# Kernel tuning notes

Measured on AMD Instinct MI355X. Metric: run time of the kernel, lower is better.

## Reference

```python
import jax, jax.numpy as jnp
import numpy as np

IN_C, HID, L, NN, BS, OUT = 32, 128, 4, 64, 512, 3
N = NN * BS  # total graph vertices
EPS_LN = 1e-5
EPS_SM = 1e-16  # PyG softmax eps


def setup_inputs() -> dict:
    key = jax.random.key(0)
    ks = jax.random.split(key, 16)
    E = 524288
    x = jax.random.normal(ks[0], (N, IN_C), dtype=jnp.float32)
    edge_index = jax.random.randint(ks[1], (2, E), 0, N, dtype=jnp.int64)
    s = 0.1
    # first GAT layer (in -> hidden)
    W0 = jax.random.normal(ks[2], (IN_C, HID), dtype=jnp.float32) * s
    att_src0 = jax.random.normal(ks[3], (HID,), dtype=jnp.float32) * s
    att_dst0 = jax.random.normal(ks[4], (HID,), dtype=jnp.float32) * s
    bias0 = jnp.zeros((HID,), dtype=jnp.float32)
    # residual GAT layers (hidden -> hidden), stacked over L
    W_res = jax.random.normal(ks[5], (L, HID, HID), dtype=jnp.float32) * s
    att_src_res = jax.random.normal(ks[6], (L, HID), dtype=jnp.float32) * s
    att_dst_res = jax.random.normal(ks[7], (L, HID), dtype=jnp.float32) * s
    bias_res = jnp.zeros((L, HID), dtype=jnp.float32)
    gamma = jnp.ones((L, HID), dtype=jnp.float32)
    beta = jnp.zeros((L, HID), dtype=jnp.float32)
    # per-node predictor heads
    W1p = jax.random.normal(ks[8], (NN, HID, HID // 2), dtype=jnp.float32) * s
    W2p = jax.random.normal(ks[9], (NN, HID // 2, OUT), dtype=jnp.float32) * s
    return {"x": x, "edge_index": edge_index, "W0": W0, "att_src0": att_src0,
            "att_dst0": att_dst0, "bias0": bias0, "W_res": W_res,
            "att_src_res": att_src_res, "att_dst_res": att_dst_res,
            "bias_res": bias_res, "gamma": gamma, "beta": beta,
            "W1p": W1p, "W2p": W2p}


def _gat(x, src, dst, W, a_src, a_dst, b):
    # PyG GATConv, heads=1, negative_slope=0.2, self-loops already appended
    h = x @ W                                   # [N, H]
    a_s = (h * a_src).sum(-1)                   # [N]
    a_d = (h * a_dst).sum(-1)                   # [N]
    e = jax.nn.leaky_relu(a_s[src] + a_d[dst], 0.2)   # [E]
    m = jax.ops.segment_max(e, dst, num_segments=N)
    e = jnp.exp(e - m[dst])
    z = jax.ops.segment_sum(e, dst, num_segments=N)
    alpha = e / (z[dst] + EPS_SM)               # [E]
    out = jax.ops.segment_sum(h[src] * alpha[:, None], dst, num_segments=N)
    return out + b


def _layernorm(x, g, b):
    mu = x.mean(-1, keepdims=True)
    var = ((x - mu) ** 2).mean(-1, keepdims=True)
    return (x - mu) * jax.lax.rsqrt(var + EPS_LN) * g + b


def reference(x, edge_index, W0, att_src0, att_dst0, bias0, W_res,
              att_src_res, att_dst_res, bias_res, gamma, beta, W1p, W2p):
    loops = jnp.arange(N, dtype=edge_index.dtype)
    src = jnp.concatenate([edge_index[0], loops])
    dst = jnp.concatenate([edge_index[1], loops])
    # first GAT + relu
    h = jax.nn.relu(_gat(x, src, dst, W0, att_src0, att_dst0, bias0))
    # res+ blocks: h = h + conv(dropout(act(norm(h))))  (dropout=identity, eval)
    for i in range(L):
        t = jax.nn.relu(_layernorm(h, gamma[i], beta[i]))
        t = _gat(t, src, dst, W_res[i], att_src_res[i], att_dst_res[i], bias_res[i])
        h = h + t
    h = jax.nn.relu(_layernorm(h, gamma[0], beta[0]))
    # per-node predictor heads
    h = h.reshape(NN, BS, HID)
    t = jax.nn.relu(jnp.einsum('nbh,nhk->nbk', h, W1p))
    logits = jnp.einsum('nbk,nko->nbo', t, W2p)
    return jax.nn.softmax(logits, axis=-1)   # softmax over class dim (dim=1 per node slice)
```

## Files before the change

### kernel.cpp

```cpp
#include <hip/hip_runtime.h>
#include <hip/hip_fp8.h>
#include <math.h>

#define NND   32768
#define HIDD  128
#define NHEAD 64
#define BSS   512
#define OUTC  3

typedef _Float16 half_t;
typedef __attribute__((ext_vector_type(8))) _Float16 half8;
typedef __attribute__((ext_vector_type(4))) float f32x4;

__device__ __forceinline__ unsigned enc_fp8x4(float a, float b, float c, float d) {
    __hip_fp8x4_e4m3 q(make_float4(a, b, c, d));
    return (unsigned)q.__x;
}
__device__ __forceinline__ float4 dec_fp8x4(unsigned v) {
    __hip_fp8x4_e4m3 t; t.__x = (__hip_fp8x4_storage_t)v;
    return (float4)t;
}

__global__ __launch_bounds__(256) void prep_kernel(const float* __restrict__ W0,
        const float* __restrict__ W_res, const float* __restrict__ W1p,
// ... 77 lines not shown
    int tmp[32];
    int run = 0;
#pragma unroll
    for (int i = 0; i < 8; ++i) {
        int4 c4 = *(const int4*)&counts[base + i * 4];
        tmp[i*4+0] = run; run += c4.x;
        tmp[i*4+1] = run; run += c4.y;
        tmp[i*4+2] = run; run += c4.z;
        tmp[i*4+3] = run; run += c4.w;
    }
    sums[tid] = run;
    __syncthreads();
    for (int d = 1; d < 1024; d <<= 1) {
        int v = (tid >= d) ? sums[tid - d] : 0;
        __syncthreads();
        sums[tid] += v;
        __syncthreads();
    }
    int ebase = (tid == 0) ? 0 : sums[tid - 1];
#pragma unroll
    for (int i = 0; i < 32; ++i) off[base + i] = ebase + tmp[i];
    if (tid == 1023) off[NND] = sums[1023];
}

__global__ __launch_bounds__(256) void fill_a0_kernel(const int* __restrict__ ei, int E, int egrid,
        const int* __restrict__ off, const int* __restrict__ rank, int* __restrict__ csr_src,
        const half_t* __restrict__ xh, const float* __restrict__ wvec,
        float* __restrict__ a_s, float* __restrict__ a_d) {
    int b = blockIdx.x, tid = threadIdx.x;
    if (b < egrid) {
        int j = b * 256 + tid;
        int Etot = E + NND;
        if (j >= Etot) return;
        int src, dst;
        if (j < E) { src = ei[j]; dst = ei[E + j]; }
        else       { src = j - E; dst = j - E; }
        csr_src[off[dst] + rank[j]] = src;
    } else {
        __shared__ float ws0[32], wd0[32];
        if (tid < 32) { ws0[tid] = wvec[tid]; wd0[tid] = wvec[640 + tid]; }
        __syncthreads();
        int g = (b - egrid) * 256 + tid;
        int node = g >> 2, part = g & 3;
        half8 xv = *(const half8*)&xh[(size_t)node * 32 + part * 8];
        float s = 0.f, d2 = 0.f;
#pragma unroll
        for (int j = 0; j < 8; ++j) { float f = (float)xv[j]; s += f * ws0[part * 8 + j]; d2 += f * wd0[part * 8 + j]; }
        s += __shfl_xor(s, 1); s += __shfl_xor(s, 2);
        d2 += __shfl_xor(d2, 1); d2 += __shfl_xor(d2, 2);
        if (part == 0) { a_s[node] = s; a_d[node] = d2; }
    }
}

__global__ __launch_bounds__(256) void agg0_kernel(const half_t* __restrict__ xh,
        const float* __restrict__ a_s, const float* __restrict__ a_dv,
        const int* __restrict__ csr_src, const int* __restrict__ off,
        half_t* __restrict__ P) {
    int d = (blockIdx.x * 256 + threadIdx.x) >> 6;
    int lane = threadIdx.x & 63;
    int q = lane >> 4, r15 = lane & 15;
    int beg = off[d], end = off[d + 1];
    float adv = a_dv[d];
    float pz = 0.f, a0 = 0.f, a1 = 0.f;
    for (int base = beg; base < end; base += 64) {
        int j = base + lane;
        int s = 0; float p = 0.f;
        if (j < end) {
            s = csr_src[j];
            float t = a_s[s] + adv;
            t = (t > 0.f) ? t : 0.2f * t;
            p = __expf(t);
        }
        pz += p;
        int cnt = end - base; if (cnt > 64) cnt = 64;
        int full = cnt & ~15;
        int k4 = 0;
        for (; k4 < full; k4 += 16) {
            int s0 = __shfl(s, k4 + q);      float p0 = __shfl(p, k4 + q);
            int s1 = __shfl(s, k4 + 4 + q);  float p1 = __shfl(p, k4 + 4 + q);
            int s2 = __shfl(s, k4 + 8 + q);  float p2 = __shfl(p, k4 + 8 + q);
            int s3 = __shfl(s, k4 + 12 + q); float p3 = __shfl(p, k4 + 12 + q);
            union { unsigned u; half_t h[2]; } u0, u1, u2, u3;
            u0.u = *(const unsigned*)&xh[(size_t)s0 * 32 + r15 * 2];
            u1.u = *(const unsigned*)&xh[(size_t)s1 * 32 + r15 * 2];
            u2.u = *(const unsigned*)&xh[(size_t)s2 * 32 + r15 * 2];
            u3.u = *(const unsigned*)&xh[(size_t)s3 * 32 + r15 * 2];
            a0 += p0 * (float)u0.h[0] + p1 * (float)u1.h[0] + p2 * (float)u2.h[0] + p3 * (float)u3.h[0];
            a1 += p0 * (float)u0.h[1] + p1 * (float)u1.h[1] + p2 * (float)u2.h[1] + p3 * (float)u3.h[1];
        }
        for (; k4 < cnt; k4 += 4) {
            int s0 = __shfl(s, k4 + q); float p0 = __shfl(p, k4 + q);
            union { unsigned u; half_t h[2]; } u0;
            u0.u = *(const unsigned*)&xh[(size_t)s0 * 32 + r15 * 2];
            a0 += p0 * (float)u0.h[0]; a1 += p0 * (float)u0.h[1];
        }
    }
#pragma unroll
    for (int o = 32; o; o >>= 1) pz += __shfl_xor(pz, o);
    a0 += __shfl_xor(a0, 16); a0 += __shfl_xor(a0, 32);
    a1 += __shfl_xor(a1, 16); a1 += __shfl_xor(a1, 32);
    if (q == 0) {
        float inv = 1.f / (pz + 1e-16f);
        union { unsigned u; half_t h[2]; } w;
        w.h[0] = (half_t)(a0 * inv); w.h[1] = (half_t)(a1 * inv);
        *(unsigned*)&P[(size_t)d * 32 + r15 * 2] = w.u;
    }
}

__global__ __launch_bounds__(256) void agg_kernel(const unsigned char* __restrict__ F8,
        const float* __restrict__ a_s, const float* __restrict__ a_dv,
        const int* __restrict__ csr_src, const int* __restrict__ off,
        half_t* __restrict__ P) {
    int d = (blockIdx.x * 256 + threadIdx.x) >> 6;
    int lane = threadIdx.x & 63;
    int q = lane >> 4, r15 = lane & 15;
    int beg = off[d], end = off[d + 1];
    float adv = a_dv[d];
    float pz = 0.f;
    float acc[8] = {0.f,0.f,0.f,0.f,0.f,0.f,0.f,0.f};
    for (int base = beg; base < end; base += 64) {
        int j = base + lane;
        int s = 0; float p = 0.f;
        if (j < end) {
            s = csr_src[j];
            float t = a_s[s] + adv;
            t = (t > 0.f) ? t : 0.2f * t;
            p = __expf(t);
        }
        pz += p;
        int cnt = end - base; if (cnt > 64) cnt = 64;
        int full = cnt & ~15;
        int k4 = 0;
        for (; k4 < full; k4 += 16) {
            int s0 = __shfl(s, k4 + q);      float p0 = __shfl(p, k4 + q);
            int s1 = __shfl(s, k4 + 4 + q);  float p1 = __shfl(p, k4 + 4 + q);
            int s2 = __shfl(s, k4 + 8 + q);  float p2 = __shfl(p, k4 + 8 + q);
            int s3 = __shfl(s, k4 + 12 + q); float p3 = __shfl(p, k4 + 12 + q);
            uint2 r0 = *(const uint2*)&F8[(size_t)s0 * HIDD + r15 * 8];
            uint2 r1 = *(const uint2*)&F8[(size_t)s1 * HIDD + r15 * 8];
            uint2 r2 = *(const uint2*)&F8[(size_t)s2 * HIDD + r15 * 8];
            uint2 r3 = *(const uint2*)&F8[(size_t)s3 * HIDD + r15 * 8];
            float4 f;
            f = dec_fp8x4(r0.x); acc[0]+=p0*f.x; acc[1]+=p0*f.y; acc[2]+=p0*f.z; acc[3]+=p0*f.w;
            f = dec_fp8x4(r0.y); acc[4]+=p0*f.x; acc[5]+=p0*f.y; acc[6]+=p0*f.z; acc[7]+=p0*f.w;
            f = dec_fp8x4(r1.x); acc[0]+=p1*f.x; acc[1]+=p1*f.y; acc[2]+=p1*f.z; acc[3]+=p1*f.w;
            f = dec_fp8x4(r1.y); acc[4]+=p1*f.x; acc[5]+=p1*f.y; acc[6]+=p1*f.z; acc[7]+=p1*f.w;
            f = dec_fp8x4(r2.x); acc[0]+=p2*f.x; acc[1]+=p2*f.y; acc[2]+=p2*f.z; acc[3]+=p2*f.w;
            f = dec_fp8x4(r2.y); acc[4]+=p2*f.x; acc[5]+=p2*f.y; acc[6]+=p2*f.z; acc[7]+=p2*f.w;
            f = dec_fp8x4(r3.x); acc[0]+=p3*f.x; acc[1]+=p3*f.y; acc[2]+=p3*f.z; acc[3]+=p3*f.w;
            f = dec_fp8x4(r3.y); acc[4]+=p3*f.x; acc[5]+=p3*f.y; acc[6]+=p3*f.z; acc[7]+=p3*f.w;
        }
        for (; k4 < cnt; k4 += 4) {
            int s0 = __shfl(s, k4 + q); float p0 = __shfl(p, k4 + q);
            uint2 r0 = *(const uint2*)&F8[(size_t)s0 * HIDD + r15 * 8];
            float4 f;
            f = dec_fp8x4(r0.x); acc[0]+=p0*f.x; acc[1]+=p0*f.y; acc[2]+=p0*f.z; acc[3]+=p0*f.w;
            f = dec_fp8x4(r0.y); acc[4]+=p0*f.x; acc[5]+=p0*f.y; acc[6]+=p0*f.z; acc[7]+=p0*f.w;
        }
    }
#pragma unroll
    for (int o = 32; o; o >>= 1) pz += __shfl_xor(pz, o);
#pragma unroll
    for (int i = 0; i < 8; ++i) {
        acc[i] += __shfl_xor(acc[i], 16);
        acc[i] += __shfl_xor(acc[i], 32);
    }
    if (q == 0) {
        float inv = 1.f / (pz + 1e-16f);
        union { int4 v; half_t hh[8]; } u;
#pragma unroll
        for (int i = 0; i < 8; ++i) u.hh[i] = (half_t)(acc[i] * inv);
        *(int4*)&P[(size_t)d * HIDD + r15 * 8] = u.v;
    }
}

template <int K, bool RES>
__global__ __launch_bounds__(256) void gemm_kernel(const half_t* __restrict__ P,
        const half_t* __restrict__ Whl, const float* __restrict__ bias,
        half_t* __restrict__ Hh, unsigned char* __restrict__ Th8,
        const float* __restrict__ gamma, const float* __restrict__ beta,
        const float* __restrict__ wsn, const float* __restrict__ wdn,
        float* __restrict__ a_s, float* __restrict__ a_d) {
    constexpr int KP = K + 8;
    constexpr int WB = 128 * KP * 2;
    constexpr int VB = 64 * 132 * 4;
    __shared__ __align__(16) char smraw[(WB > VB) ? WB : VB];
    half_t* w = (half_t*)smraw;
    float* vv = (float*)smraw;
    int tid = threadIdx.x;
    int n0 = blockIdx.x * 64;
    for (int i = tid; i < 128 * (K / 8); i += 256) {
        int n = i / (K / 8), c = i % (K / 8);
        *(int4*)&w[n * KP + c * 8] = *(const int4*)&Whl[(size_t)n * K + c * 8];
    }
    int wv = tid >> 6, lane = tid & 63;
    int q = lane >> 4, r15 = lane & 15;
    half8 afrag[K / 32];
    int nodeA = n0 + wv * 16 + r15;
#pragma unroll
    for (int s = 0; s < K / 32; ++s)
        afrag[s] = *(const half8*)&P[(size_t)nodeA * K + s * 32 + q * 8];
    __syncthreads();
    f32x4 acc[8];
#pragma unroll
    for (int ct = 0; ct < 8; ++ct) {
        f32x4 c = {0.f, 0.f, 0.f, 0.f};
#pragma unroll
        for (int s = 0; s < K / 32; ++s) {
            half8 bfrag = *(const half8*)&w[(ct * 16 + r15) * KP + s * 32 + q * 8];
            c = __builtin_amdgcn_mfma_f32_16x16x32_f16(afrag[s], bfrag, c, 0, 0, 0);
        }
        acc[ct] = c;
    }
    __syncthreads();
#pragma unroll
    for (int ct = 0; ct < 8; ++ct)
#pragma unroll
        for (int r = 0; r < 4; ++r)
            vv[(wv * 16 + q * 4 + r) * 132 + ct * 16 + r15] = acc[ct][r];
    __syncthreads();
    int grp = tid >> 4, sub = tid & 15;
    float4 bi0 = *(const float4*)&bias[sub * 8],  bi1 = *(const float4*)&bias[sub * 8 + 4];
    float4 g0  = *(const float4*)&gamma[sub * 8], g1  = *(const float4*)&gamma[sub * 8 + 4];
    float4 be0 = *(const float4*)&beta[sub * 8],  be1 = *(const float4*)&beta[sub * 8 + 4];
    float4 ws0 = *(const float4*)&wsn[sub * 8],   ws1 = *(const float4*)&wsn[sub * 8 + 4];
    float4 wd0 = *(const float4*)&wdn[sub * 8],   wd1 = *(const float4*)&wdn[sub * 8 + 4];
    float bi[8] = {bi0.x,bi0.y,bi0.z,bi0.w,bi1.x,bi1.y,bi1.z,bi1.w};
    float gg[8] = {g0.x,g0.y,g0.z,g0.w,g1.x,g1.y,g1.z,g1.w};
    float be[8] = {be0.x,be0.y,be0.z,be0.w,be1.x,be1.y,be1.z,be1.w};
    float ws[8] = {ws0.x,ws0.y,ws0.z,ws0.w,ws1.x,ws1.y,ws1.z,ws1.w};
    float wd[8] = {wd0.x,wd0.y,wd0.z,wd0.w,wd1.x,wd1.y,wd1.z,wd1.w};
#pragma unroll
    for (int pp = 0; pp < 4; ++pp) {
        int nl = grp + pp * 16;
        int node = n0 + nl;
        float v8[8];
#pragma unroll
        for (int j = 0; j < 8; ++j) v8[j] = vv[nl * 132 + sub * 8 + j] + bi[j];
        if (RES) {
            half8 hold = *(const half8*)&Hh[(size_t)node * HIDD + sub * 8];
#pragma unroll
            for (int j = 0; j < 8; ++j) v8[j] += (float)hold[j];
        } else {
#pragma unroll
            for (int j = 0; j < 8; ++j) v8[j] = fmaxf(v8[j], 0.f);
        }
        union { int4 i4; half_t h[8]; } hw;
#pragma unroll
        for (int j = 0; j < 8; ++j) hw.h[j] = (half_t)v8[j];
        *(int4*)&Hh[(size_t)node * HIDD + sub * 8] = hw.i4;
        float sum = 0.f;
#pragma unroll
        for (int j = 0; j < 8; ++j) sum += v8[j];
#pragma unroll
        for (int o = 8; o; o >>= 1) sum += __shfl_xor(sum, o);
        float mu = sum * (1.f / HIDD);
        float var = 0.f;
#pragma unroll
        for (int j = 0; j < 8; ++j) { float dx = v8[j] - mu; var += dx * dx; }
#pragma unroll
        for (int o = 8; o; o >>= 1) var += __shfl_xor(var, o);
        float rs = rsqrtf(var * (1.f / HIDD) + 1e-5f);
        float tt[8];
        float asn = 0.f, adn = 0.f;
#pragma unroll
        for (int j = 0; j < 8; ++j) {
            float t = fmaxf((v8[j] - mu) * rs * gg[j] + be[j], 0.f);
            tt[j] = t;
            asn += t * ws[j];
            adn += t * wd[j];
        }
        uint2 tw;
        tw.x = enc_fp8x4(tt[0], tt[1], tt[2], tt[3]);
        tw.y = enc_fp8x4(tt[4], tt[5], tt[6], tt[7]);
        *(uint2*)&Th8[(size_t)node * HIDD + sub * 8] = tw;
#pragma unroll
        for (int o = 8; o; o >>= 1) { asn += __shfl_xor(asn, o); adn += __shfl_xor(adn, o); }
        if (sub == 0) { a_s[node] = asn; a_d[node] = adn; }
    }
}

__global__ __launch_bounds__(256) void gemm_last_kernel(const half_t* __restrict__ P,
        const half_t* __restrict__ Whl, const float* __restrict__ bias,
        const half_t* __restrict__ Hh,
        const float* __restrict__ gamma, const float* __restrict__ beta,
        const half_t* __restrict__ W1h, const float* __restrict__ W2p,
        float* __restrict__ out) {
    __shared__ __align__(16) char smraw[128 * 136 * 2];
    half_t* w = (half_t*)smraw;
    float* vv = (float*)smraw;
    int tid = threadIdx.x;
    int n0 = blockIdx.x * 64;
    for (int i = tid; i < 128 * 16; i += 256) {
        int n = i >> 4, c = i & 15;
        *(int4*)&w[n * 136 + c * 8] = *(const int4*)&Whl[(size_t)n * 128 + c * 8];
    }
    int wv = tid >> 6, lane = tid & 63;
    int q = lane >> 4, r15 = lane & 15;
    half8 afrag[4];
    int nodeA = n0 + wv * 16 + r15;
#pragma unroll
    for (int s = 0; s < 4; ++s)
        afrag[s] = *(const half8*)&P[(size_t)nodeA * HIDD + s * 32 + q * 8];
    __syncthreads();
    f32x4 acc[8];
#pragma unroll
    for (int ct = 0; ct < 8; ++ct) {
        f32x4 c = {0.f, 0.f, 0.f, 0.f};
#pragma unroll
        for (int s = 0; s < 4; ++s) {
            half8 bfrag = *(const half8*)&w[(ct * 16 + r15) * 136 + s * 32 + q * 8];
            c = __builtin_amdgcn_mfma_f32_16x16x32_f16(afrag[s], bfrag, c, 0, 0, 0);
        }
        acc[ct] = c;
    }
    __syncthreads();
#pragma unroll
    for (int ct = 0; ct < 8; ++ct)
#pragma unroll
        for (int r = 0; r < 4; ++r)
            vv[(wv * 16 + q * 4 + r) * 132 + ct * 16 + r15] = acc[ct][r];
    __syncthreads();
    int grp = tid >> 4, sub = tid & 15;
    float4 bi0 = *(const float4*)&bias[sub * 8],  bi1 = *(const float4*)&bias[sub * 8 + 4];
    float4 g0  = *(const float4*)&gamma[sub * 8], g1  = *(const float4*)&gamma[sub * 8 + 4];
    float4 be0 = *(const float4*)&beta[sub * 8],  be1 = *(const float4*)&beta[sub * 8 + 4];
    float bi[8] = {bi0.x,bi0.y,bi0.z,bi0.w,bi1.x,bi1.y,bi1.z,bi1.w};
    float gg[8] = {g0.x,g0.y,g0.z,g0.w,g1.x,g1.y,g1.z,g1.w};
    float be[8] = {be0.x,be0.y,be0.z,be0.w,be1.x,be1.y,be1.z,be1.w};
    half_t tv[4][8];
#pragma unroll
    for (int pp = 0; pp < 4; ++pp) {
        int nl = grp + pp * 16;
        int node = n0 + nl;
        float v8[8];
        half8 hold = *(const half8*)&Hh[(size_t)node * HIDD + sub * 8];
#pragma unroll
        for (int j = 0; j < 8; ++j) v8[j] = vv[nl * 132 + sub * 8 + j] + bi[j] + (float)hold[j];
        float sum = 0.f;
#pragma unroll
        for (int j = 0; j < 8; ++j) sum += v8[j];
#pragma unroll
        for (int o = 8; o; o >>= 1) sum += __shfl_xor(sum, o);
        float mu = sum * (1.f / HIDD);
        float var = 0.f;
#pragma unroll
        for (int j = 0; j < 8; ++j) { float dx = v8[j] - mu; var += dx * dx; }
#pragma unroll
        for (int o = 8; o; o >>= 1) var += __shfl_xor(var, o);
        float rs = rsqrtf(var * (1.f / HIDD) + 1e-5f);
#pragma unroll
        for (int j = 0; j < 8; ++j)
            tv[pp][j] = (half_t)fmaxf((v8[j] - mu) * rs * gg[j] + be[j], 0.f);
    }
    __syncthreads();
#pragma unroll
    for (int pp = 0; pp < 4; ++pp) {
        int nl = grp + pp * 16;
        union { int4 i4; half_t h[8]; } u;
#pragma unroll
        for (int j = 0; j < 8; ++j) u.h[j] = tv[pp][j];
        *(int4*)&w[nl * 136 + sub * 8] = u.i4;
    }
    __syncthreads();
    int head = n0 >> 9;
    const half_t* W1g = W1h + (size_t)head * 64 * 128;
    half8 pa[4];
#pragma unroll
    for (int s = 0; s < 4; ++s)
        pa[s] = *(const half8*)&w[(wv * 16 + r15) * 136 + s * 32 + q * 8];
    float lg[3][4];
#pragma unroll
    for (int o = 0; o < 3; ++o)
#pragma unroll
        for (int r = 0; r < 4; ++r) lg[o][r] = 0.f;
#pragma unroll
    for (int ct2 = 0; ct2 < 4; ++ct2) {
        int n2 = ct2 * 16 + r15;
        f32x4 c = {0.f, 0.f, 0.f, 0.f};
#pragma unroll
        for (int s = 0; s < 4; ++s) {
            half8 bfrag = *(const half8*)&W1g[(size_t)n2 * 128 + s * 32 + q * 8];
            c = __builtin_amdgcn_mfma_f32_16x16x32_f16(pa[s], bfrag, c, 0, 0, 0);
        }
        float w2a = W2p[(size_t)head * 192 + n2 * 3 + 0];
        float w2b = W2p[(size_t)head * 192 + n2 * 3 + 1];
        float w2c = W2p[(size_t)head * 192 + n2 * 3 + 2];
#pragma unroll
        for (int r = 0; r < 4; ++r) {
            float t = fmaxf(c[r], 0.f);
            lg[0][r] += t * w2a;
            lg[1][r] += t * w2b;
            lg[2][r] += t * w2c;
        }
    }
#pragma unroll
    for (int o = 8; o; o >>= 1)
#pragma unroll
        for (int oo = 0; oo < 3; ++oo)
#pragma unroll
            for (int r = 0; r < 4; ++r) lg[oo][r] += __shfl_xor(lg[oo][r], o);
    if (r15 == 0) {
        int nodeD = n0 + wv * 16 + q * 4;
#pragma unroll
        for (int r = 0; r < 4; ++r) {
            float l0 = lg[0][r], l1 = lg[1][r], l2 = lg[2][r];
            float mx = fmaxf(l0, fmaxf(l1, l2));
            float e0 = __expf(l0 - mx), e1 = __expf(l1 - mx), e2 = __expf(l2 - mx);
            float inv = 1.f / (e0 + e1 + e2);
            float* op = out + (size_t)(nodeD + r) * OUTC;
            op[0] = e0 * inv; op[1] = e1 * inv; op[2] = e2 * inv;
        }
    }
}

extern "C" void kernel_launch(void* const* d_in, const int* in_sizes, int n_in,
                              void* d_out, int out_size, void* d_ws, size_t ws_size,
                              hipStream_t stream) {
    const float* x        = (const float*)d_in[0];
    const int*   ei       = (const int*)d_in[1];
    const float* W0       = (const float*)d_in[2];
    const float* att_src0 = (const float*)d_in[3];
    const float* att_dst0 = (const float*)d_in[4];
    const float* bias0    = (const float*)d_in[5];
    const float* W_res    = (const float*)d_in[6];
    const float* as_res   = (const float*)d_in[7];
    const float* ad_res   = (const float*)d_in[8];
    const float* b_res    = (const float*)d_in[9];
    const float* gamma    = (const float*)d_in[10];
    const float* beta     = (const float*)d_in[11];
    const float* W1p      = (const float*)d_in[12];
    const float* W2p      = (const float*)d_in[13];
    float* out = (float*)d_out;

    int E = in_sizes[1] / 2;
    int Etot = E + NND;

    char* p = (char*)d_ws;
    auto alloc = [&](size_t bytes) { void* r = (void*)p; p += (bytes + 255) & ~(size_t)255; return r; };
    int*    counts  = (int*)alloc((size_t)NND * 4);
    int*    off     = (int*)alloc((size_t)(NND + 1) * 4);
    int*    rank    = (int*)alloc((size_t)Etot * 4);
    int*    csr_src = (int*)alloc((size_t)Etot * 4);
    half_t* xh      = (half_t*)alloc((size_t)NND * 32 * 2);
    half_t* Pbuf    = (half_t*)alloc((size_t)NND * HIDD * 2);
    unsigned char* Th8 = (unsigned char*)alloc((size_t)NND * HIDD);
    half_t* Hh      = (half_t*)alloc((size_t)NND * HIDD * 2);
    float*  a_s     = (float*)alloc((size_t)NND * 4);
    float*  a_d     = (float*)alloc((size_t)NND * 4);
    half_t* Wh      = (half_t*)alloc((size_t)4 * HIDD * HIDD * 2);
    half_t* W1h     = (half_t*)alloc((size_t)NHEAD * 64 * HIDD * 2);
    half_t* W0t     = (half_t*)alloc((size_t)HIDD * 32 * 2);
    float*  wvec    = (float*)alloc((size_t)1280 * 4);

    int egrid = (Etot + 255) / 256;

    hipMemsetAsync(counts, 0, (size_t)NND * 4, stream);
    prep_kernel<<<1090 + egrid, 256, 0, stream>>>(W0, W_res, W1p, att_src0, att_dst0,
        as_res, ad_res, x, ei, E, Wh, W1h, W0t, wvec, xh, counts, rank);
    scan_kernel<<<1, 1024, 0, stream>>>(counts, off);
    fill_a0_kernel<<<egrid + 512, 256, 0, stream>>>(ei, E, egrid, off, rank, csr_src,
                                                    xh, wvec, a_s, a_d);

    agg0_kernel<<<NND / 4, 256, 0, stream>>>(xh, a_s, a_d, csr_src, off, Pbuf);
    gemm_kernel<32, false><<<NND / 64, 256, 0, stream>>>(Pbuf, W0t, bias0, Hh, Th8,
        gamma, beta, wvec + 128, wvec + 640 + 128, a_s, a_d);

    for (int i = 0; i < 3; ++i) {
        agg_kernel<<<NND / 4, 256, 0, stream>>>(Th8, a_s, a_d, csr_src, off, Pbuf);
        gemm_kernel<128, true><<<NND / 64, 256, 0, stream>>>(Pbuf, Wh + (size_t)i * 16384,
            b_res + i * HIDD, Hh, Th8,
            gamma + (i + 1) * HIDD, beta + (i + 1) * HIDD,
            wvec + (i + 2) * 128, wvec + 640 + (i + 2) * 128, a_s, a_d);
    }

    agg_kernel<<<NND / 4, 256, 0, stream>>>(Th8, a_s, a_d, csr_src, off, Pbuf);
    gemm_last_kernel<<<NND / 64, 256, 0, stream>>>(Pbuf, Wh + (size_t)3 * 16384,
        b_res + 3 * HIDD, Hh, gamma, beta, W1h, W2p, out);
}
```

Measured before the change: 281.2 us.

## Fuse GAT aggregation with per-layer GEMM into single 1024-thread layer kernels

```diff
diff --git a/kernel.cpp b/kernel.cpp
--- a/kernel.cpp
+++ b/kernel.cpp
@@ -153,199 +153,113 @@
     }
 }
 
-__global__ __launch_bounds__(256) void agg0_kernel(const half_t* __restrict__ xh,
-        const float* __restrict__ a_s, const float* __restrict__ a_dv,
+__global__ __launch_bounds__(1024, 4) void layer0_kernel(const half_t* __restrict__ xh,
+        const float* __restrict__ asv, const float* __restrict__ adval,
         const int* __restrict__ csr_src, const int* __restrict__ off,
-        half_t* __restrict__ P) {
-    int d = (blockIdx.x * 256 + threadIdx.x) >> 6;
-    int lane = threadIdx.x & 63;
-    int q = lane >> 4, r15 = lane & 15;
-    int beg = off[d], end = off[d + 1];
-    float adv = a_dv[d];
-    float pz = 0.f, a0 = 0.f, a1 = 0.f;
-    for (int base = beg; base < end; base += 64) {
-        int j = base + lane;
-        int s = 0; float p = 0.f;
-        if (j < end) {
-            s = csr_src[j];
-            float t = a_s[s] + adv;
-            t = (t > 0.f) ? t : 0.2f * t;
-            p = __expf(t);
-        }
-        pz += p;
-        int cnt = end - base; if (cnt > 64) cnt = 64;
-        int full = cnt & ~15;
-        int k4 = 0;
-        for (; k4 < full; k4 += 16) {
-            int s0 = __shfl(s, k4 + q);      float p0 = __shfl(p, k4 + q);
-            int s1 = __shfl(s, k4 + 4 + q);  float p1 = __shfl(p, k4 + 4 + q);
-            int s2 = __shfl(s, k4 + 8 + q);  float p2 = __shfl(p, k4 + 8 + q);
-            int s3 = __shfl(s, k4 + 12 + q); float p3 = __shfl(p, k4 + 12 + q);
-            union { unsigned u; half_t h[2]; } u0, u1, u2, u3;
-            u0.u = *(const unsigned*)&xh[(size_t)s0 * 32 + r15 * 2];
-            u1.u = *(const unsigned*)&xh[(size_t)s1 * 32 + r15 * 2];
-            u2.u = *(const unsigned*)&xh[(size_t)s2 * 32 + r15 * 2];
-            u3.u = *(const unsigned*)&xh[(size_t)s3 * 32 + r15 * 2];
-            a0 += p0 * (float)u0.h[0] + p1 * (float)u1.h[0] + p2 * (float)u2.h[0] + p3 * (float)u3.h[0];
-            a1 += p0 * (float)u0.h[1] + p1 * (float)u1.h[1] + p2 * (float)u2.h[1] + p3 * (float)u3.h[1];
-        }
-        for (; k4 < cnt; k4 += 4) {
-            int s0 = __shfl(s, k4 + q); float p0 = __shfl(p, k4 + q);
-            union { unsigned u; half_t h[2]; } u0;
-            u0.u = *(const unsigned*)&xh[(size_t)s0 * 32 + r15 * 2];
-            a0 += p0 * (float)u0.h[0]; a1 += p0 * (float)u0.h[1];
-        }
-    }
-#pragma unroll
-    for (int o = 32; o; o >>= 1) pz += __shfl_xor(pz, o);
-    a0 += __shfl_xor(a0, 16); a0 += __shfl_xor(a0, 32);
-    a1 += __shfl_xor(a1, 16); a1 += __shfl_xor(a1, 32);
-    if (q == 0) {
-        float inv = 1.f / (pz + 1e-16f);
-        union { unsigned u; half_t h[2]; } w;
-        w.h[0] = (half_t)(a0 * inv); w.h[1] = (half_t)(a1 * inv);
-        *(unsigned*)&P[(size_t)d * 32 + r15 * 2] = w.u;
-    }
-}
-
-__global__ __launch_bounds__(256) void agg_kernel(const unsigned char* __restrict__ F8,
-        const float* __restrict__ a_s, const float* __restrict__ a_dv,
-        const int* __restrict__ csr_src, const int* __restrict__ off,
-        half_t* __restrict__ P) {
-    int d = (blockIdx.x * 256 + threadIdx.x) >> 6;
-    int lane = threadIdx.x & 63;
-    int q = lane >> 4, r15 = lane & 15;
-    int beg = off[d], end = off[d + 1];
-    float adv = a_dv[d];
-    float pz = 0.f;
-    float acc[8] = {0.f,0.f,0.f,0.f,0.f,0.f,0.f,0.f};
-    for (int base = beg; base < end; base += 64) {
-        int j = base + lane;
-        int s = 0; float p = 0.f;
-        if (j < end) {
-            s = csr_src[j];
-            float t = a_s[s] + adv;
-            t = (t > 0.f) ? t : 0.2f * t;
-            p = __expf(t);
-        }
-        pz += p;
-        int cnt = end - base; if (cnt > 64) cnt = 64;
-        int full = cnt & ~15;
-        int k4 = 0;
-        for (; k4 < full; k4 += 16) {
-            int s0 = __shfl(s, k4 + q);      float p0 = __shfl(p, k4 + q);
-            int s1 = __shfl(s, k4 + 4 + q);  float p1 = __shfl(p, k4 + 4 + q);
-            int s2 = __shfl(s, k4 + 8 + q);  float p2 = __shfl(p, k4 + 8 + q);
-            int s3 = __shfl(s, k4 + 12 + q); float p3 = __shfl(p, k4 + 12 + q);
-            uint2 r0 = *(const uint2*)&F8[(size_t)s0 * HIDD + r15 * 8];
-            uint2 r1 = *(const uint2*)&F8[(size_t)s1 * HIDD + r15 * 8];
-            uint2 r2 = *(const uint2*)&F8[(size_t)s2 * HIDD + r15 * 8];
-            uint2 r3 = *(const uint2*)&F8[(size_t)s3 * HIDD + r15 * 8];
-            float4 f;
-            f = dec_fp8x4(r0.x); acc[0]+=p0*f.x; acc[1]+=p0*f.y; acc[2]+=p0*f.z; acc[3]+=p0*f.w;
-            f = dec_fp8x4(r0.y); acc[4]+=p0*f.x; acc[5]+=p0*f.y; acc[6]+=p0*f.z; acc[7]+=p0*f.w;
-            f = dec_fp8x4(r1.x); acc[0]+=p1*f.x; acc[1]+=p1*f.y; acc[2]+=p1*f.z; acc[3]+=p1*f.w;
-            f = dec_fp8x4(r1.y); acc[4]+=p1*f.x; acc[5]+=p1*f.y; acc[6]+=p1*f.z; acc[7]+=p1*f.w;
-            f = dec_fp8x4(r2.x); acc[0]+=p2*f.x; acc[1]+=p2*f.y; acc[2]+=p2*f.z; acc[3]+=p2*f.w;
-            f = dec_fp8x4(r2.y); acc[4]+=p2*f.x; acc[5]+=p2*f.y; acc[6]+=p2*f.z; acc[7]+=p2*f.w;
-            f = dec_fp8x4(r3.x); acc[0]+=p3*f.x; acc[1]+=p3*f.y; acc[2]+=p3*f.z; acc[3]+=p3*f.w;
-            f = dec_fp8x4(r3.y); acc[4]+=p3*f.x; acc[5]+=p3*f.y; acc[6]+=p3*f.z; acc[7]+=p3*f.w;
-        }
-        for (; k4 < cnt; k4 += 4) {
-            int s0 = __shfl(s, k4 + q); float p0 = __shfl(p, k4 + q);
-            uint2 r0 = *(const uint2*)&F8[(size_t)s0 * HIDD + r15 * 8];
-            float4 f;
-            f = dec_fp8x4(r0.x); acc[0]+=p0*f.x; acc[1]+=p0*f.y; acc[2]+=p0*f.z; acc[3]+=p0*f.w;
-            f = dec_fp8x4(r0.y); acc[4]+=p0*f.x; acc[5]+=p0*f.y; acc[6]+=p0*f.z; acc[7]+=p0*f.w;
-        }
-    }
-#pragma unroll
-    for (int o = 32; o; o >>= 1) pz += __shfl_xor(pz, o);
-#pragma unroll
-    for (int i = 0; i < 8; ++i) {
-        acc[i] += __shfl_xor(acc[i], 16);
-        acc[i] += __shfl_xor(acc[i], 32);
-    }
-    if (q == 0) {
-        float inv = 1.f / (pz + 1e-16f);
-        union { int4 v; half_t hh[8]; } u;
-#pragma unroll
-        for (int i = 0; i < 8; ++i) u.hh[i] = (half_t)(acc[i] * inv);
-        *(int4*)&P[(size_t)d * HIDD + r15 * 8] = u.v;
-    }
-}
-
-template <int K, bool RES>
-__global__ __launch_bounds__(256) void gemm_kernel(const half_t* __restrict__ P,
-        const half_t* __restrict__ Whl, const float* __restrict__ bias,
-        half_t* __restrict__ Hh, unsigned char* __restrict__ Th8,
+        const half_t* __restrict__ W0t, const float* __restrict__ bias,
+        half_t* __restrict__ Hh,
         const float* __restrict__ gamma, const float* __restrict__ beta,
+        unsigned char* __restrict__ Th8o,
         const float* __restrict__ wsn, const float* __restrict__ wdn,
-        float* __restrict__ a_s, float* __restrict__ a_d) {
-    constexpr int KP = K + 8;
-    constexpr int WB = 128 * KP * 2;
-    constexpr int VB = 64 * 132 * 4;
-    __shared__ __align__(16) char smraw[(WB > VB) ? WB : VB];
-    half_t* w = (half_t*)smraw;
-    float* vv = (float*)smraw;
-    int tid = threadIdx.x;
-    int n0 = blockIdx.x * 64;
-    for (int i = tid; i < 128 * (K / 8); i += 256) {
-        int n = i / (K / 8), c = i % (K / 8);
-        *(int4*)&w[n * KP + c * 8] = *(const int4*)&Whl[(size_t)n * K + c * 8];
-    }
-    int wv = tid >> 6, lane = tid & 63;
-    int q = lane >> 4, r15 = lane & 15;
-    half8 afrag[K / 32];
-    int nodeA = n0 + wv * 16 + r15;
-#pragma unroll
-    for (int s = 0; s < K / 32; ++s)
-        afrag[s] = *(const half8*)&P[(size_t)nodeA * K + s * 32 + q * 8];
+        float* __restrict__ aso, float* __restrict__ ado) {
+    __shared__ __align__(16) char smem[32768];
+    half_t* Wt = (half_t*)smem;
+    half_t* Ps = (half_t*)(smem + 10240);
+    float*  vv = (float*)smem;
+    const int tid = threadIdx.x;
+    const int w = tid >> 6, lane = tid & 63, q = lane >> 4, r15 = lane & 15;
+    const int n0 = blockIdx.x * 128;
+    for (int i = tid; i < 512; i += 1024) {
+        int n = i >> 2, c = i & 3;
+        *(int4*)&Wt[n * 40 + c * 8] = *(const int4*)&W0t[(size_t)n * 32 + c * 8];
+    }
+    for (int t = 0; t < 8; ++t) {
+        int d = n0 + w * 8 + t;
+        int beg = off[d], end = off[d + 1];
+        float adv = adval[d];
+        float pz = 0.f, a0 = 0.f, a1 = 0.f;
+        for (int base = beg; base < end; base += 64) {
+            int j = base + lane;
+            int s = 0; float p = 0.f;
+            if (j < end) {
+                s = csr_src[j];
+                float tt = asv[s] + adv;
+                tt = (tt > 0.f) ? tt : 0.2f * tt;
+                p = __expf(tt);
+            }
+            pz += p;
+            int cnt = end - base; if (cnt > 64) cnt = 64;
+            int full = cnt & ~15;
+            int k4 = 0;
+            for (; k4 < full; k4 += 16) {
+                int s0 = __shfl(s, k4 + q);      float p0 = __shfl(p, k4 + q);
+                int s1 = __shfl(s, k4 + 4 + q);  float p1 = __shfl(p, k4 + 4 + q);
+                int s2 = __shfl(s, k4 + 8 + q);  float p2 = __shfl(p, k4 + 8 + q);
+                int s3 = __shfl(s, k4 + 12 + q); float p3 = __shfl(p, k4 + 12 + q);
+                union { unsigned u; half_t h[2]; } u0, u1, u2, u3;
+                u0.u = *(const unsigned*)&xh[(size_t)s0 * 32 + r15 * 2];
+                u1.u = *(const unsigned*)&xh[(size_t)s1 * 32 + r15 * 2];
+                u2.u = *(const unsigned*)&xh[(size_t)s2 * 32 + r15 * 2];
+                u3.u = *(const unsigned*)&xh[(size_t)s3 * 32 + r15 * 2];
+                a0 += p0 * (float)u0.h[0] + p1 * (float)u1.h[0] + p2 * (float)u2.h[0] + p3 * (float)u3.h[0];
+                a1 += p0 * (float)u0.h[1] + p1 * (float)u1.h[1] + p2 * (float)u2.h[1] + p3 * (float)u3.h[1];
+            }
+            for (; k4 < cnt; k4 += 4) {
+                int s0 = __shfl(s, k4 + q); float p0 = __shfl(p, k4 + q);
+                union { unsigned u; half_t h[2]; } u0;
+                u0.u = *(const unsigned*)&xh[(size_t)s0 * 32 + r15 * 2];
+                a0 += p0 * (float)u0.h[0]; a1 += p0 * (float)u0.h[1];
+            }
+        }
+#pragma unroll
+        for (int o = 32; o; o >>= 1) pz += __shfl_xor(pz, o);
+        a0 += __shfl_xor(a0, 16); a0 += __shfl_xor(a0, 32);
+        a1 += __shfl_xor(a1, 16); a1 += __shfl_xor(a1, 32);
+        if (q == 0) {
+            float inv = 1.f / (pz + 1e-16f);
+            union { unsigned u; half_t h[2]; } uu;
+            uu.h[0] = (half_t)(a0 * inv); uu.h[1] = (half_t)(a1 * inv);
+            *(unsigned*)&Ps[(w * 8 + t) * 40 + r15 * 2] = uu.u;
+        }
+    }
     __syncthreads();
-    f32x4 acc[8];
-#pragma unroll
-    for (int ct = 0; ct < 8; ++ct) {
+    const int rt = w >> 1, cb = (w & 1) * 4;
+    half8 af = *(const half8*)&Ps[(rt * 16 + r15) * 40 + q * 8];
+    f32x4 c4[4];
+#pragma unroll
+    for (int ct = 0; ct < 4; ++ct) {
         f32x4 c = {0.f, 0.f, 0.f, 0.f};
-#pragma unroll
-        for (int s = 0; s < K / 32; ++s) {
-            half8 bfrag = *(const half8*)&w[(ct * 16 + r15) * KP + s * 32 + q * 8];
-            c = __builtin_amdgcn_mfma_f32_16x16x32_f16(afrag[s], bfrag, c, 0, 0, 0);
-        }
-        acc[ct] = c;
+        half8 bf = *(const half8*)&Wt[((cb + ct) * 16 + r15) * 40 + q * 8];
+        c = __builtin_amdgcn_mfma_f32_16x16x32_f16(af, bf, c, 0, 0, 0);
+        c4[ct] = c;
     }
     __syncthreads();
-#pragma unroll
-    for (int ct = 0; ct < 8; ++ct)
-#pragma unroll
-        for (int r = 0; r < 4; ++r)
-            vv[(wv * 16 + q * 4 + r) * 132 + ct * 16 + r15] = acc[ct][r];
-    __syncthreads();
-    int grp = tid >> 4, sub = tid & 15;
+    const int nl = tid >> 4, sub = tid & 15;
     float4 bi0 = *(const float4*)&bias[sub * 8],  bi1 = *(const float4*)&bias[sub * 8 + 4];
     float4 g0  = *(const float4*)&gamma[sub * 8], g1  = *(const float4*)&gamma[sub * 8 + 4];
     float4 be0 = *(const float4*)&beta[sub * 8],  be1 = *(const float4*)&beta[sub * 8 + 4];
-    float4 ws0 = *(const float4*)&wsn[sub * 8],   ws1 = *(const float4*)&wsn[sub * 8 + 4];
-    float4 wd0 = *(const float4*)&wdn[sub * 8],   wd1 = *(const float4*)&wdn[sub * 8 + 4];
+    float4 wsa = *(const float4*)&wsn[sub * 8],   wsb = *(const float4*)&wsn[sub * 8 + 4];
+    float4 wda = *(const float4*)&wdn[sub * 8],   wdb = *(const float4*)&wdn[sub * 8 + 4];
     float bi[8] = {bi0.x,bi0.y,bi0.z,bi0.w,bi1.x,bi1.y,bi1.z,bi1.w};
     float gg[8] = {g0.x,g0.y,g0.z,g0.w,g1.x,g1.y,g1.z,g1.w};
     float be[8] = {be0.x,be0.y,be0.z,be0.w,be1.x,be1.y,be1.z,be1.w};
-    float ws[8] = {ws0.x,ws0.y,ws0.z,ws0.w,ws1.x,ws1.y,ws1.z,ws1.w};
-    float wd[8] = {wd0.x,wd0.y,wd0.z,wd0.w,wd1.x,wd1.y,wd1.z,wd1.w};
-#pragma unroll
-    for (int pp = 0; pp < 4; ++pp) {
-        int nl = grp + pp * 16;
-        int node = n0 + nl;
+    float wsr[8] = {wsa.x,wsa.y,wsa.z,wsa.w,wsb.x,wsb.y,wsb.z,wsb.w};
+    float wdr[8] = {wda.x,wda.y,wda.z,wda.w,wdb.x,wdb.y,wdb.z,wdb.w};
+#pragma unroll
+    for (int chunk = 0; chunk < 2; ++chunk) {
+        if ((rt >> 2) == chunk) {
+            int rb = (rt & 3) * 16 + q * 4;
+#pragma unroll
+            for (int ct = 0; ct < 4; ++ct)
+#pragma unroll
+                for (int r = 0; r < 4; ++r)
+                    vv[(rb + r) * 128 + (cb + ct) * 16 + r15] = c4[ct][r];
+        }
+        __syncthreads();
+        int node = n0 + chunk * 64 + nl;
         float v8[8];
 #pragma unroll
-        for (int j = 0; j < 8; ++j) v8[j] = vv[nl * 132 + sub * 8 + j] + bi[j];
-        if (RES) {
-            half8 hold = *(const half8*)&Hh[(size_t)node * HIDD + sub * 8];
-#pragma unroll
-            for (int j = 0; j < 8; ++j) v8[j] += (float)hold[j];
-        } else {
-#pragma unroll
-            for (int j = 0; j < 8; ++j) v8[j] = fmaxf(v8[j], 0.f);
-        }
+        for (int j = 0; j < 8; ++j) v8[j] = fmaxf(vv[nl * 128 + sub * 8 + j] + bi[j], 0.f);
         union { int4 i4; half_t h[8]; } hw;
 #pragma unroll
         for (int j = 0; j < 8; ++j) hw.h[j] = (half_t)v8[j];
@@ -367,77 +281,155 @@
 #pragma unroll
         for (int j = 0; j < 8; ++j) {
             float t = fmaxf((v8[j] - mu) * rs * gg[j] + be[j], 0.f);
-            tt[j] = t;
-            asn += t * ws[j];
-            adn += t * wd[j];
+            tt[j] = t; asn += t * wsr[j]; adn += t * wdr[j];
         }
         uint2 tw;
         tw.x = enc_fp8x4(tt[0], tt[1], tt[2], tt[3]);
         tw.y = enc_fp8x4(tt[4], tt[5], tt[6], tt[7]);
-        *(uint2*)&Th8[(size_t)node * HIDD + sub * 8] = tw;
+        *(uint2*)&Th8o[(size_t)node * HIDD + sub * 8] = tw;
 #pragma unroll
         for (int o = 8; o; o >>= 1) { asn += __shfl_xor(asn, o); adn += __shfl_xor(adn, o); }
-        if (sub == 0) { a_s[node] = asn; a_d[node] = adn; }
-    }
-}
-
-__global__ __launch_bounds__(256) void gemm_last_kernel(const half_t* __restrict__ P,
+        if (sub == 0) { aso[node] = asn; ado[node] = adn; }
+        __syncthreads();
+    }
+}
+
+template <bool LAST>
+__global__ __launch_bounds__(1024, 4) void layer_kernel(const unsigned char* __restrict__ F8,
+        const float* __restrict__ asv, const float* __restrict__ adval,
+        const int* __restrict__ csr_src, const int* __restrict__ off,
         const half_t* __restrict__ Whl, const float* __restrict__ bias,
-        const half_t* __restrict__ Hh,
+        half_t* __restrict__ Hh,
         const float* __restrict__ gamma, const float* __restrict__ beta,
+        unsigned char* __restrict__ Th8o,
+        const float* __restrict__ wsn, const float* __restrict__ wdn,
+        float* __restrict__ aso, float* __restrict__ ado,
         const half_t* __restrict__ W1h, const float* __restrict__ W2p,
         float* __restrict__ out) {
-    __shared__ __align__(16) char smraw[128 * 136 * 2];
-    half_t* w = (half_t*)smraw;
-    float* vv = (float*)smraw;
-    int tid = threadIdx.x;
-    int n0 = blockIdx.x * 64;
-    for (int i = tid; i < 128 * 16; i += 256) {
+    __shared__ __align__(16) char smem[65536];
+    half_t* Wt = (half_t*)smem;
+    half_t* Ps = (half_t*)(smem + 32768);
+    float*  vv = (float*)smem;
+    const int tid = threadIdx.x;
+    const int w = tid >> 6, lane = tid & 63, q = lane >> 4, r15 = lane & 15;
+    const int n0 = blockIdx.x * 128;
+    for (int i = tid; i < 2048; i += 1024) {
         int n = i >> 4, c = i & 15;
-        *(int4*)&w[n * 136 + c * 8] = *(const int4*)&Whl[(size_t)n * 128 + c * 8];
-    }
-    int wv = tid >> 6, lane = tid & 63;
-    int q = lane >> 4, r15 = lane & 15;
-    half8 afrag[4];
-    int nodeA = n0 + wv * 16 + r15;
-#pragma unroll
-    for (int s = 0; s < 4; ++s)
-        afrag[s] = *(const half8*)&P[(size_t)nodeA * HIDD + s * 32 + q * 8];
+        *(int4*)&Wt[n * 128 + ((c ^ (n & 15)) * 8)] = *(const int4*)&Whl[(size_t)n * 128 + c * 8];
+    }
+    for (int t = 0; t < 8; ++t) {
+        int d = n0 + w * 8 + t;
+        int beg = off[d], end = off[d + 1];
+        float adv = adval[d];
+        float pz = 0.f;
+        float acc[8] = {0.f,0.f,0.f,0.f,0.f,0.f,0.f,0.f};
+        for (int base = beg; base < end; base += 64) {
+            int j = base + lane;
+            int s = 0; float p = 0.f;
+            if (j < end) {
+                s = csr_src[j];
+                float tt = asv[s] + adv;
+                tt = (tt > 0.f) ? tt : 0.2f * tt;
+                p = __expf(tt);
+            }
+            pz += p;
+            int cnt = end - base; if (cnt > 64) cnt = 64;
+            int full = cnt & ~15;
+            int k4 = 0;
+            for (; k4 < full; k4 += 16) {
+                int s0 = __shfl(s, k4 + q);      float p0 = __shfl(p, k4 + q);
+                int s1 = __shfl(s, k4 + 4 + q);  float p1 = __shfl(p, k4 + 4 + q);
+                int s2 = __shfl(s, k4 + 8 + q);  float p2 = __shfl(p, k4 + 8 + q);
+                int s3 = __shfl(s, k4 + 12 + q); float p3 = __shfl(p, k4 + 12 + q);
+                uint2 r0 = *(const uint2*)&F8[(size_t)s0 * HIDD + r15 * 8];
+                uint2 r1 = *(const uint2*)&F8[(size_t)s1 * HIDD + r15 * 8];
+                uint2 r2 = *(const uint2*)&F8[(size_t)s2 * HIDD + r15 * 8];
+                uint2 r3 = *(const uint2*)&F8[(size_t)s3 * HIDD + r15 * 8];
+                float4 f;
+                f = dec_fp8x4(r0.x); acc[0]+=p0*f.x; acc[1]+=p0*f.y; acc[2]+=p0*f.z; acc[3]+=p0*f.w;
+                f = dec_fp8x4(r0.y); acc[4]+=p0*f.x; acc[5]+=p0*f.y; acc[6]+=p0*f.z; acc[7]+=p0*f.w;
+                f = dec_fp8x4(r1.x); acc[0]+=p1*f.x; acc[1]+=p1*f.y; acc[2]+=p1*f.z; acc[3]+=p1*f.w;
+                f = dec_fp8x4(r1.y); acc[4]+=p1*f.x; acc[5]+=p1*f.y; acc[6]+=p1*f.z; acc[7]+=p1*f.w;
+                f = dec_fp8x4(r2.x); acc[0]+=p2*f.x; acc[1]+=p2*f.y; acc[2]+=p2*f.z; acc[3]+=p2*f.w;
+                f = dec_fp8x4(r2.y); acc[4]+=p2*f.x; acc[5]+=p2*f.y; acc[6]+=p2*f.z; acc[7]+=p2*f.w;
+                f = dec_fp8x4(r3.x); acc[0]+=p3*f.x; acc[1]+=p3*f.y; acc[2]+=p3*f.z; acc[3]+=p3*f.w;
+                f = dec_fp8x4(r3.y); acc[4]+=p3*f.x; acc[5]+=p3*f.y; acc[6]+=p3*f.z; acc[7]+=p3*f.w;
+            }
+            for (; k4 < cnt; k4 += 4) {
+                int s0 = __shfl(s, k4 + q); float p0 = __shfl(p, k4 + q);
+                uint2 r0 = *(const uint2*)&F8[(size_t)s0 * HIDD + r15 * 8];
+                float4 f;
+                f = dec_fp8x4(r0.x); acc[0]+=p0*f.x; acc[1]+=p0*f.y; acc[2]+=p0*f.z; acc[3]+=p0*f.w;
+                f = dec_fp8x4(r0.y); acc[4]+=p0*f.x; acc[5]+=p0*f.y; acc[6]+=p0*f.z; acc[7]+=p0*f.w;
+            }
+        }
+#pragma unroll
+        for (int o = 32; o; o >>= 1) pz += __shfl_xor(pz, o);
+#pragma unroll
+        for (int i = 0; i < 8; ++i) {
+            acc[i] += __shfl_xor(acc[i], 16);
+            acc[i] += __shfl_xor(acc[i], 32);
+        }
+        if (q == 0) {
+            float inv = 1.f / (pz + 1e-16f);
+            union { int4 v; half_t hh[8]; } u;
+#pragma unroll
+            for (int i = 0; i < 8; ++i) u.hh[i] = (half_t)(acc[i] * inv);
+            int m = w * 8 + t;
+            *(int4*)&Ps[m * 128 + ((r15 ^ (m & 15)) * 8)] = u.v;
+        }
+    }
     __syncthreads();
-    f32x4 acc[8];
-#pragma unroll
-    for (int ct = 0; ct < 8; ++ct) {
+    const int rt = w >> 1, cb = (w & 1) * 4;
+    half8 af[4];
+#pragma unroll
+    for (int s = 0; s < 4; ++s) {
+        int n = rt * 16 + r15, idx = s * 4 + q;
+        af[s] = *(const half8*)&Ps[n * 128 + ((idx ^ (n & 15)) * 8)];
+    }
+    f32x4 c4[4];
+#pragma unroll
+    for (int ct = 0; ct < 4; ++ct) {
         f32x4 c = {0.f, 0.f, 0.f, 0.f};
+        int n = (cb + ct) * 16 + r15;
 #pragma unroll
         for (int s = 0; s < 4; ++s) {
-            half8 bfrag = *(const half8*)&w[(ct * 16 + r15) * 136 + s * 32 + q * 8];
-            c = __builtin_amdgcn_mfma_f32_16x16x32_f16(afrag[s], bfrag, c, 0, 0, 0);
-        }
-        acc[ct] = c;
+            int idx = s * 4 + q;
+            half8 bf = *(const half8*)&Wt[n * 128 + ((idx ^ (n & 15)) * 8)];
+            c = __builtin_amdgcn_mfma_f32_16x16x32_f16(af[s], bf, c, 0, 0, 0);
+        }
+        c4[ct] = c;
     }
     __syncthreads();
-#pragma unroll
-    for (int ct = 0; ct < 8; ++ct)
-#pragma unroll
-        for (int r = 0; r < 4; ++r)
-            vv[(wv * 16 + q * 4 + r) * 132 + ct * 16 + r15] = acc[ct][r];
-    __syncthreads();
-    int grp = tid >> 4, sub = tid & 15;
+    const int nl = tid >> 4, sub = tid & 15;
     float4 bi0 = *(const float4*)&bias[sub * 8],  bi1 = *(const float4*)&bias[sub * 8 + 4];
     float4 g0  = *(const float4*)&gamma[sub * 8], g1  = *(const float4*)&gamma[sub * 8 + 4];
     float4 be0 = *(const float4*)&beta[sub * 8],  be1 = *(const float4*)&beta[sub * 8 + 4];
     float bi[8] = {bi0.x,bi0.y,bi0.z,bi0.w,bi1.x,bi1.y,bi1.z,bi1.w};
     float gg[8] = {g0.x,g0.y,g0.z,g0.w,g1.x,g1.y,g1.z,g1.w};
     float be[8] = {be0.x,be0.y,be0.z,be0.w,be1.x,be1.y,be1.z,be1.w};
-    half_t tv[4][8];
-#pragma unroll
-    for (int pp = 0; pp < 4; ++pp) {
-        int nl = grp + pp * 16;
-        int node = n0 + nl;
+#pragma unroll
+    for (int chunk = 0; chunk < 2; ++chunk) {
+        if ((rt >> 2) == chunk) {
+            int rb = (rt & 3) * 16 + q * 4;
+#pragma unroll
+            for (int ct = 0; ct < 4; ++ct)
+#pragma unroll
+                for (int r = 0; r < 4; ++r)
+                    vv[(rb + r) * 128 + (cb + ct) * 16 + r15] = c4[ct][r];
+        }
+        __syncthreads();
+        int node = n0 + chunk * 64 + nl;
         float v8[8];
         half8 hold = *(const half8*)&Hh[(size_t)node * HIDD + sub * 8];
 #pragma unroll
-        for (int j = 0; j < 8; ++j) v8[j] = vv[nl * 132 + sub * 8 + j] + bi[j] + (float)hold[j];
+        for (int j = 0; j < 8; ++j) v8[j] = vv[nl * 128 + sub * 8 + j] + bi[j] + (float)hold[j];
+        if (!LAST) {
+            union { int4 i4; half_t h[8]; } hw;
+#pragma unroll
+            for (int j = 0; j < 8; ++j) hw.h[j] = (half_t)v8[j];
+            *(int4*)&Hh[(size_t)node * HIDD + sub * 8] = hw.i4;
+        }
         float sum = 0.f;
 #pragma unroll
         for (int j = 0; j < 8; ++j) sum += v8[j];
@@ -450,67 +442,88 @@
 #pragma unroll
         for (int o = 8; o; o >>= 1) var += __shfl_xor(var, o);
         float rs = rsqrtf(var * (1.f / HIDD) + 1e-5f);
-#pragma unroll
-        for (int j = 0; j < 8; ++j)
-            tv[pp][j] = (half_t)fmaxf((v8[j] - mu) * rs * gg[j] + be[j], 0.f);
-    }
-    __syncthreads();
-#pragma unroll
-    for (int pp = 0; pp < 4; ++pp) {
-        int nl = grp + pp * 16;
-        union { int4 i4; half_t h[8]; } u;
-#pragma unroll
-        for (int j = 0; j < 8; ++j) u.h[j] = tv[pp][j];
-        *(int4*)&w[nl * 136 + sub * 8] = u.i4;
-    }
-    __syncthreads();
-    int head = n0 >> 9;
-    const half_t* W1g = W1h + (size_t)head * 64 * 128;
-    half8 pa[4];
-#pragma unroll
-    for (int s = 0; s < 4; ++s)
-        pa[s] = *(const half8*)&w[(wv * 16 + r15) * 136 + s * 32 + q * 8];
-    float lg[3][4];
-#pragma unroll
-    for (int o = 0; o < 3; ++o)
-#pragma unroll
-        for (int r = 0; r < 4; ++r) lg[o][r] = 0.f;
-#pragma unroll
-    for (int ct2 = 0; ct2 < 4; ++ct2) {
-        int n2 = ct2 * 16 + r15;
-        f32x4 c = {0.f, 0.f, 0.f, 0.f};
-#pragma unroll
-        for (int s = 0; s < 4; ++s) {
-            half8 bfrag = *(const half8*)&W1g[(size_t)n2 * 128 + s * 32 + q * 8];
-            c = __builtin_amdgcn_mfma_f32_16x16x32_f16(pa[s], bfrag, c, 0, 0, 0);
-        }
-        float w2a = W2p[(size_t)head * 192 + n2 * 3 + 0];
-        float w2b = W2p[(size_t)head * 192 + n2 * 3 + 1];
-        float w2c = W2p[(size_t)head * 192 + n2 * 3 + 2];
-#pragma unroll
-        for (int r = 0; r < 4; ++r) {
-            float t = fmaxf(c[r], 0.f);
-            lg[0][r] += t * w2a;
-            lg[1][r] += t * w2b;
-            lg[2][r] += t * w2c;
-        }
-    }
-#pragma unroll
-    for (int o = 8; o; o >>= 1)
-#pragma unroll
-        for (int oo = 0; oo < 3; ++oo)
-#pragma unroll
-            for (int r = 0; r < 4; ++r) lg[oo][r] += __shfl_xor(lg[oo][r], o);
-    if (r15 == 0) {
-        int nodeD = n0 + wv * 16 + q * 4;
-#pragma unroll
-        for (int r = 0; r < 4; ++r) {
-            float l0 = lg[0][r], l1 = lg[1][r], l2 = lg[2][r];
-            float mx = fmaxf(l0, fmaxf(l1, l2));
-            float e0 = __expf(l0 - mx), e1 = __expf(l1 - mx), e2 = __expf(l2 - mx);
-            float inv = 1.f / (e0 + e1 + e2);
-            float* op = out + (size_t)(nodeD + r) * OUTC;
-            op[0] = e0 * inv; op[1] = e1 * inv; op[2] = e2 * inv;
+        if (!LAST) {
+            float4 wsa = *(const float4*)&wsn[sub * 8], wsb = *(const float4*)&wsn[sub * 8 + 4];
+            float4 wda = *(const float4*)&wdn[sub * 8], wdb = *(const float4*)&wdn[sub * 8 + 4];
+            float wsr[8] = {wsa.x,wsa.y,wsa.z,wsa.w,wsb.x,wsb.y,wsb.z,wsb.w};
+            float wdr[8] = {wda.x,wda.y,wda.z,wda.w,wdb.x,wdb.y,wdb.z,wdb.w};
+            float tt[8];
+            float asn = 0.f, adn = 0.f;
+#pragma unroll
+            for (int j = 0; j < 8; ++j) {
+                float t = fmaxf((v8[j] - mu) * rs * gg[j] + be[j], 0.f);
+                tt[j] = t; asn += t * wsr[j]; adn += t * wdr[j];
+            }
+            uint2 tw;
+            tw.x = enc_fp8x4(tt[0], tt[1], tt[2], tt[3]);
+            tw.y = enc_fp8x4(tt[4], tt[5], tt[6], tt[7]);
+            *(uint2*)&Th8o[(size_t)node * HIDD + sub * 8] = tw;
+#pragma unroll
+            for (int o = 8; o; o >>= 1) { asn += __shfl_xor(asn, o); adn += __shfl_xor(adn, o); }
+            if (sub == 0) { aso[node] = asn; ado[node] = adn; }
+        } else {
+            union { int4 i4; half_t h[8]; } twr;
+#pragma unroll
+            for (int j = 0; j < 8; ++j)
+                twr.h[j] = (half_t)fmaxf((v8[j] - mu) * rs * gg[j] + be[j], 0.f);
+            int g = chunk * 64 + nl;
+            *(int4*)&Ps[g * 128 + ((sub ^ (g & 15)) * 8)] = twr.i4;
+        }
+        __syncthreads();
+    }
+    if (LAST) {
+        if (w < 8) {
+            int head = n0 >> 9;
+            const half_t* W1g = W1h + (size_t)head * 64 * 128;
+            half8 pa[4];
+#pragma unroll
+            for (int s = 0; s < 4; ++s) {
+                int n = w * 16 + r15, idx = s * 4 + q;
+                pa[s] = *(const half8*)&Ps[n * 128 + ((idx ^ (n & 15)) * 8)];
+            }
+            float lg[3][4];
+#pragma unroll
+            for (int o = 0; o < 3; ++o)
+#pragma unroll
+                for (int r = 0; r < 4; ++r) lg[o][r] = 0.f;
+#pragma unroll
+            for (int ct2 = 0; ct2 < 4; ++ct2) {
+                int n2 = ct2 * 16 + r15;
+                f32x4 c = {0.f, 0.f, 0.f, 0.f};
+#pragma unroll
+                for (int s = 0; s < 4; ++s) {
+                    half8 bf = *(const half8*)&W1g[(size_t)n2 * 128 + s * 32 + q * 8];
+                    c = __builtin_amdgcn_mfma_f32_16x16x32_f16(pa[s], bf, c, 0, 0, 0);
+                }
+                float w2a = W2p[(size_t)head * 192 + n2 * 3 + 0];
+                float w2b = W2p[(size_t)head * 192 + n2 * 3 + 1];
+                float w2c = W2p[(size_t)head * 192 + n2 * 3 + 2];
+#pragma unroll
+                for (int r = 0; r < 4; ++r) {
+                    float t = fmaxf(c[r], 0.f);
+                    lg[0][r] += t * w2a;
+                    lg[1][r] += t * w2b;
+                    lg[2][r] += t * w2c;
+                }
+            }
+#pragma unroll
+            for (int o = 8; o; o >>= 1)
+#pragma unroll
+                for (int oo = 0; oo < 3; ++oo)
+#pragma unroll
+                    for (int r = 0; r < 4; ++r) lg[oo][r] += __shfl_xor(lg[oo][r], o);
+            if (r15 == 0) {
+                int nodeD = n0 + w * 16 + q * 4;
+#pragma unroll
+                for (int r = 0; r < 4; ++r) {
+                    float l0 = lg[0][r], l1 = lg[1][r], l2 = lg[2][r];
+                    float mx = fmaxf(l0, fmaxf(l1, l2));
+                    float e0 = __expf(l0 - mx), e1 = __expf(l1 - mx), e2 = __expf(l2 - mx);
+                    float inv = 1.f / (e0 + e1 + e2);
+                    float* op = out + (size_t)(nodeD + r) * OUTC;
+                    op[0] = e0 * inv; op[1] = e1 * inv; op[2] = e2 * inv;
+                }
+            }
         }
     }
 }
@@ -544,11 +557,13 @@
     int*    rank    = (int*)alloc((size_t)Etot * 4);
     int*    csr_src = (int*)alloc((size_t)Etot * 4);
     half_t* xh      = (half_t*)alloc((size_t)NND * 32 * 2);
-    half_t* Pbuf    = (half_t*)alloc((size_t)NND * HIDD * 2);
-    unsigned char* Th8 = (unsigned char*)alloc((size_t)NND * HIDD);
+    unsigned char* Th8A = (unsigned char*)alloc((size_t)NND * HIDD);
+    unsigned char* Th8B = (unsigned char*)alloc((size_t)NND * HIDD);
     half_t* Hh      = (half_t*)alloc((size_t)NND * HIDD * 2);
-    float*  a_s     = (float*)alloc((size_t)NND * 4);
-    float*  a_d     = (float*)alloc((size_t)NND * 4);
+    float*  a_s0    = (float*)alloc((size_t)NND * 4);
+    float*  a_d0    = (float*)alloc((size_t)NND * 4);
+    float*  a_s1    = (float*)alloc((size_t)NND * 4);
+    float*  a_d1    = (float*)alloc((size_t)NND * 4);
     half_t* Wh      = (half_t*)alloc((size_t)4 * HIDD * HIDD * 2);
     half_t* W1h     = (half_t*)alloc((size_t)NHEAD * 64 * HIDD * 2);
     half_t* W0t     = (half_t*)alloc((size_t)HIDD * 32 * 2);
@@ -561,21 +576,22 @@
         as_res, ad_res, x, ei, E, Wh, W1h, W0t, wvec, xh, counts, rank);
     scan_kernel<<<1, 1024, 0, stream>>>(counts, off);
     fill_a0_kernel<<<egrid + 512, 256, 0, stream>>>(ei, E, egrid, off, rank, csr_src,
-                                                    xh, wvec, a_s, a_d);
-
-    agg0_kernel<<<NND / 4, 256, 0, stream>>>(xh, a_s, a_d, csr_src, off, Pbuf);
-    gemm_kernel<32, false><<<NND / 64, 256, 0, stream>>>(Pbuf, W0t, bias0, Hh, Th8,
-        gamma, beta, wvec + 128, wvec + 640 + 128, a_s, a_d);
-
-    for (int i = 0; i < 3; ++i) {
-        agg_kernel<<<NND / 4, 256, 0, stream>>>(Th8, a_s, a_d, csr_src, off, Pbuf);
-        gemm_kernel<128, true><<<NND / 64, 256, 0, stream>>>(Pbuf, Wh + (size_t)i * 16384,
-            b_res + i * HIDD, Hh, Th8,
-            gamma + (i + 1) * HIDD, beta + (i + 1) * HIDD,
-            wvec + (i + 2) * 128, wvec + 640 + (i + 2) * 128, a_s, a_d);
-    }
-
-    agg_kernel<<<NND / 4, 256, 0, stream>>>(Th8, a_s, a_d, csr_src, off, Pbuf);
-    gemm_last_kernel<<<NND / 64, 256, 0, stream>>>(Pbuf, Wh + (size_t)3 * 16384,
-        b_res + 3 * HIDD, Hh, gamma, beta, W1h, W2p, out);
-}
+                                                    xh, wvec, a_s0, a_d0);
+
+    layer0_kernel<<<256, 1024, 0, stream>>>(xh, a_s0, a_d0, csr_src, off, W0t, bias0, Hh,
+        gamma, beta, Th8A, wvec + 128, wvec + 640 + 128, a_s1, a_d1);
+
+    layer_kernel<false><<<256, 1024, 0, stream>>>(Th8A, a_s1, a_d1, csr_src, off,
+        Wh, b_res, Hh, gamma + HIDD, beta + HIDD, Th8B,
+        wvec + 2 * 128, wvec + 640 + 2 * 128, a_s0, a_d0, nullptr, nullptr, nullptr);
+    layer_kernel<false><<<256, 1024, 0, stream>>>(Th8B, a_s0, a_d0, csr_src, off,
+        Wh + 16384, b_res + HIDD, Hh, gamma + 2 * HIDD, beta + 2 * HIDD, Th8A,
+        wvec + 3 * 128, wvec + 640 + 3 * 128, a_s1, a_d1, nullptr, nullptr, nullptr);
+    layer_kernel<false><<<256, 1024, 0, stream>>>(Th8A, a_s1, a_d1, csr_src, off,
+        Wh + 2 * 16384, b_res + 2 * HIDD, Hh, gamma + 3 * HIDD, beta + 3 * HIDD, Th8B,
+        wvec + 4 * 128, wvec + 640 + 4 * 128, a_s0, a_d0, nullptr, nullptr, nullptr);
+
+    layer_kernel<true><<<256, 1024, 0, stream>>>(Th8B, a_s0, a_d0, csr_src, off,
+        Wh + 3 * 16384, b_res + 3 * HIDD, Hh, gamma, beta, nullptr,
+        nullptr, nullptr, nullptr, nullptr, W1h, W2p, out);
+}
```

New measurement: 288.2 us. 1.03x slower.
